# Performance work log

Measured on AMD Instinct MI355X. Metric: run time of the kernel, lower is better.

## Reference

```python
import jax, jax.numpy as jnp
import numpy as np
from jax import lax

N_FREE = 10
DT = 0.1
COMP = 4


def setup_inputs() -> dict:
    key = jax.random.key(0)
    kx, kw = jax.random.split(key)
    B, D = 256, 16384
    nodes = D // COMP  # 4096
    x = jax.random.normal(kx, (B, D), dtype=jnp.float32)
    # Hopfield-style node-coupling matrix (learned parameter), small init for stable relaxation
    W = jax.random.normal(kw, (nodes, nodes), dtype=jnp.float32) * 0.02
    return {"x": x, "W": W}


def reference(x, W):
    B, D = x.shape
    nodes = D // COMP
    # project scalar features to multivectors (B, nodes, comp)
    x_mv = x.reshape(B, nodes, COMP)
    W_sym = 0.5 * (W + W.T)  # symmetric coupling => well-defined energy

    def step(h, _):
        rho = jnp.tanh(h)                                      # (B, nodes, comp)
        drive = jnp.einsum('nm,bmc->bnc', W_sym, rho) + x_mv   # recurrent + input coupling
        grad_E = h - (1.0 - rho * rho) * drive                 # dE/dh
        return h - DT * grad_E, None

    h_free, _ = lax.scan(step, x_mv, None, length=N_FREE)
    return h_free[..., 0]  # scalar (grade-0) component, (B, nodes)
```

## Files before the change

### kernel.cpp

```cpp
#include <hip/hip_runtime.h>
#include <hip/hip_bf16.h>


#define NODES 4096
#define KDIM  4096
#define MDIM  1024
#define DLEN  16384
#define HALF_ELEMS 4194304

typedef __attribute__((ext_vector_type(8))) __bf16 bf16x8;
typedef __attribute__((ext_vector_type(8))) unsigned short u16x8;
typedef __attribute__((ext_vector_type(4))) float  f32x4;

static __device__ __forceinline__ unsigned short f32_to_bf16(float f) {
    unsigned int u = __float_as_uint(f);
    u += 0x7fffu + ((u >> 16) & 1u);
    return (unsigned short)(u >> 16);
}
static __device__ __forceinline__ float bf16_to_f32(unsigned short u) {
    return __uint_as_float(((unsigned int)u) << 16);
}

__global__ __launch_bounds__(256)
void symw_kernel(const float* __restrict__ W, unsigned short* __restrict__ Wbp) {
    __shared__ float Ta[64][64];
    __shared__ float Tb[64][65];
    const int tn = blockIdx.y, tm = blockIdx.x;
    const int c  = threadIdx.x & 63;
    const int r0 = threadIdx.x >> 6;
#pragma unroll
    for (int rr = 0; rr < 16; ++rr) {
        int r = r0 * 16 + rr;
        Ta[r][c] = W[(size_t)(tn * 64 + r) * 4096 + tm * 64 + c];
        Tb[r][c] = W[(size_t)(tm * 64 + r) * 4096 + tn * 64 + c];
    }
    __syncthreads();
#pragma unroll
    for (int rr = 0; rr < 16; ++rr) {
        int r = r0 * 16 + rr;
        float v = 0.5f * (Ta[r][c] + Tb[c][r]);
        int n = tn * 64 + r;
        int k = tm * 64 + c;
        size_t addr = ((size_t)(k >> 5) * 256 + (n >> 4)) * 512
                    + (size_t)((n & 15) | (((k >> 3) & 3) << 4)) * 8 + (k & 7);
        Wbp[addr] = f32_to_bf16(v);
    }
}

__global__ __launch_bounds__(256)
void init_kernel(const float* __restrict__ x, float* __restrict__ h,
                 unsigned short* __restrict__ P0) {
    int idx = blockIdx.x * blockDim.x + threadIdx.x;
    int b = idx >> 12;
    int m = idx & 4095;
    f32x4 xv = *(const f32x4*)(x + (size_t)idx * 4);
    *(f32x4*)(h + (size_t)idx * 4) = xv;
    size_t base = ((size_t)(m >> 5) * 64 + (b >> 2)) * 512
                + (size_t)((m >> 3) & 3) * 128 + (m & 7);
#pragma unroll
    for (int c = 0; c < 4; ++c) {
        P0[base + (size_t)((b & 3) * 4 + c) * 8] = f32_to_bf16(tanhf(xv[c]));
    }
}

__global__ __launch_bounds__(256, 4)
void gemm_kernel(const unsigned short* __restrict__ Pcur,
                 const unsigned short* __restrict__ Wbp,
                 unsigned short* __restrict__ Dp) {
    __shared__ unsigned short Bs[4 * 4096];

    const int id   = blockIdx.x;
    const int bx   = (id & 7) * 4 + ((id >> 3) & 3);
    const int by   = (id >> 5) & 7;
    const int ks   = id >> 8;
    const int T0   = ks * 32;

    const int tid  = threadIdx.x;
    const int w    = tid >> 6;
    const int lane = tid & 63;
    const int wm   = w >> 1;
    const int wn   = w & 1;

    size_t soff[2]; int dsto[2];
#pragma unroll
    for (int j = 0; j < 2; ++j) {
        int c = tid + 256 * j;
        soff[j] = ((size_t)(bx * 8 + (c >> 6))) * 512 + (size_t)(c & 63) * 8;
        dsto[j] = c * 8;
    }
    size_t aoff[4];
#pragma unroll
    for (int mi = 0; mi < 4; ++mi)
        aoff[mi] = ((size_t)(by * 8 + wm * 4 + mi)) * 512 + (size_t)lane * 8;
    const int boff = (wn * 4) * 512 + lane * 8;

    f32x4 acc[4][4];
#pragma unroll
    for (int mi = 0; mi < 4; ++mi)
#pragma unroll
        for (int ni = 0; ni < 4; ++ni)
            acc[mi][ni] = (f32x4){0.f, 0.f, 0.f, 0.f};

    bf16x8 aA[4], aB[4];

#define TC(t) ((t) < 31 ? (t) : 31)

#define STAGE(slot, tl)                                                         \
    do {                                                                        \
        const unsigned short* src = Wbp + (size_t)(T0 + (tl)) * 131072;         \
        _Pragma("unroll")                                                       \
        for (int j = 0; j < 2; ++j) {                                           \
            __builtin_amdgcn_global_load_lds(                                   \
                (const __attribute__((address_space(1))) void*)(src + soff[j]), \
                (__attribute__((address_space(3))) void*)                      \
                    (Bs + (slot) * 4096 + dsto[j]),                             \
                16, 0, 0);                                                      \
        }                                                                       \
    } while (0)

#define LOADA(s, tl)                                                            \
    do {                                                                        \
        const unsigned short* Pt = Pcur + (size_t)(T0 + (tl)) * 32768;          \
        _Pragma("unroll")                                                       \
        for (int mi = 0; mi < 4; ++mi)                                          \
            s[mi] = *(const bf16x8*)(Pt + aoff[mi]);                            \
    } while (0)

#define COMPUTE(slot, s)                                                        \
    do {                                                                        \
        const unsigned short* Bb = Bs + (slot) * 4096;                          \
        bf16x8 bfr[4];                                                          \
        _Pragma("unroll")                                                       \
        for (int ni = 0; ni < 4; ++ni)                                          \
            bfr[ni] = *(const bf16x8*)(Bb + boff + ni * 512);                   \
        _Pragma("unroll")                                                       \
        for (int mi = 0; mi < 4; ++mi)                                          \
            _Pragma("unroll")                                                   \
            for (int ni = 0; ni < 4; ++ni)                                      \
                acc[mi][ni] = __builtin_amdgcn_mfma_f32_16x16x32_bf16(          \
                    s[mi], bfr[ni], acc[mi][ni], 0, 0, 0);                      \
    } while (0)

    STAGE(0, 0);
    LOADA(aA, 0);
    STAGE(1, 1);
    STAGE(2, 2);
    LOADA(aB, 1);
    STAGE(3, 3);
    asm volatile("s_waitcnt vmcnt(10)" ::: "memory");
    __builtin_amdgcn_s_barrier();
    COMPUTE(0, aA);

    for (int tp = 0; tp < 15; ++tp) {
        const int t = 1 + 2 * tp;
        LOADA(aA, TC(t + 1));
        STAGE((t + 3) & 3, TC(t + 3));
        asm volatile("s_waitcnt vmcnt(10)" ::: "memory");
        __builtin_amdgcn_s_barrier();
        COMPUTE(t & 3, aB);

        const int u = t + 1;
        LOADA(aB, TC(u + 1));
        STAGE((u + 3) & 3, TC(u + 3));
        asm volatile("s_waitcnt vmcnt(10)" ::: "memory");
        __builtin_amdgcn_s_barrier();
        COMPUTE(u & 3, aA);
    }
    asm volatile("s_waitcnt vmcnt(0)" ::: "memory");
    __builtin_amdgcn_s_barrier();
    COMPUTE(31 & 3, aB);
#undef STAGE
#undef LOADA
#undef COMPUTE
#undef TC

    const int lr = lane & 15, lk = lane >> 4;
    unsigned short* D = Dp + (size_t)ks * HALF_ELEMS;
#pragma unroll
    for (int mi = 0; mi < 4; ++mi) {
        int i0 = by * 128 + wm * 64 + mi * 16 + lk * 4;
#pragma unroll
        for (int ni = 0; ni < 4; ++ni) {
            int n = bx * 128 + wn * 64 + ni * 16 + lr;
#pragma unroll
            for (int r = 0; r < 4; ++r)
                D[(size_t)(i0 + r) * NODES + n] = f32_to_bf16(acc[mi][ni][r]);
        }
    }
}

__global__ __launch_bounds__(256)
void combine_kernel(const unsigned short* __restrict__ Dp,
                    const float* __restrict__ x,
                    float* __restrict__ h,
                    unsigned short* __restrict__ Pnxt,
                    float* __restrict__ out) {
    int g  = blockIdx.x * 256 + threadIdx.x;
    int b  = g >> 9;
    int mg = (g & 511) << 3;
    size_t hbase = (size_t)b * DLEN + (size_t)mg * 4;

    f32x4 hv[8], xv[8];
#pragma unroll
    for (int e = 0; e < 8; ++e) {
        hv[e] = *(const f32x4*)(h + hbase + e * 4);
        xv[e] = *(const f32x4*)(x + hbase + e * 4);
    }
    u16x8 d0[4], d1[4], d2[4], d3[4];
#pragma unroll
    for (int c = 0; c < 4; ++c) {
        size_t off = (size_t)(b * 4 + c) * NODES + mg;
        d0[c] = *(const u16x8*)(Dp + off);
        d1[c] = *(const u16x8*)(Dp + HALF_ELEMS + off);
        d2[c] = *(const u16x8*)(Dp + 2 * (size_t)HALF_ELEMS + off);
        d3[c] = *(const u16x8*)(Dp + 3 * (size_t)HALF_ELEMS + off);
    }
    u16x8 pn[4];
    float o[8];
#pragma unroll
    for (int e = 0; e < 8; ++e) {
#pragma unroll
        for (int c = 0; c < 4; ++c) {
            float p = (bf16_to_f32(d0[c][e]) + bf16_to_f32(d1[c][e]))
                    + (bf16_to_f32(d2[c][e]) + bf16_to_f32(d3[c][e]));
            float hvv  = hv[e][c];
            float rho  = tanhf(hvv);
            float drive = p + xv[e][c];
            float hnew = 0.9f * hvv + 0.1f * (1.0f - rho * rho) * drive;
            hv[e][c] = hnew;
            pn[c][e] = f32_to_bf16(tanhf(hnew));
            if (c == 0) o[e] = hnew;
        }
    }
    if (Pnxt) {
#pragma unroll
        for (int e = 0; e < 8; ++e)
            *(f32x4*)(h + hbase + e * 4) = hv[e];
#pragma unroll
        for (int c = 0; c < 4; ++c) {
            size_t pa = (size_t)(mg >> 5) * 32768 + (size_t)(b >> 2) * 512
                      + (size_t)(((b & 3) * 4 + c) | (((mg >> 3) & 3) << 4)) * 8;
            *(u16x8*)(Pnxt + pa) = pn[c];
        }
    }
    if (out) {
        *(f32x4*)(out + (size_t)b * NODES + mg)     = (f32x4){o[0], o[1], o[2], o[3]};
        *(f32x4*)(out + (size_t)b * NODES + mg + 4) = (f32x4){o[4], o[5], o[6], o[7]};
    }
}

extern "C" void kernel_launch(void* const* d_in, const int* in_sizes, int n_in,
                              void* d_out, int out_size, void* d_ws, size_t ws_size,
                              hipStream_t stream) {
    const float* x = (const float*)d_in[0];
    const float* W = (const float*)d_in[1];
    float* out = (float*)d_out;

    char* ws = (char*)d_ws;
    unsigned short* Wbp = (unsigned short*)(ws);
    unsigned short* P0  = (unsigned short*)(ws + ((size_t)32 << 20));
    unsigned short* P1  = (unsigned short*)(ws + ((size_t)40 << 20));
    float*          h   = (float*)(ws + ((size_t)48 << 20));
    unsigned short* Dp  = (unsigned short*)(ws + ((size_t)64 << 20));

    symw_kernel<<<dim3(64, 64), 256, 0, stream>>>(W, Wbp);
    init_kernel<<<dim3(4096), 256, 0, stream>>>(x, h, P0);

    unsigned short* pc = P0;
    unsigned short* pn = P1;
    for (int s = 0; s < 10; ++s) {
        gemm_kernel<<<dim3(1024), 256, 0, stream>>>(pc, Wbp, Dp);
        combine_kernel<<<dim3(512), 256, 0, stream>>>(
            Dp, x, h, (s == 9) ? nullptr : pn, (s == 9) ? out : nullptr);
        unsigned short* t = pc; pc = pn; pn = t;
    }
}
```

Baseline: 645.8 us.

## Restructure GEMM to 512-thread blocks with 2-way split-K and triple-buffered LDS

The GEMM moves from 1024 blocks of 256 threads with 4-way split-K to 256 blocks of 512 threads with 2-way split-K. Each block now covers a 256-row tile, and each stage loads two K-slices into a triple-buffered LDS ring. MFMA phases are wrapped in s_setprio, and the combine kernel now sums two partials instead of four. The aim is to cut partial-sum traffic and raise reuse per block. The cost is exactly one block per CU (256 blocks), which gives less latency hiding and a longer serial K loop.

Result: faster. 618.4 us (-4.2%).

```diff
diff --git a/kernel.cpp b/kernel.cpp
--- a/kernel.cpp
+++ b/kernel.cpp
@@ -63,17 +63,16 @@
     }
 }
 
-__global__ __launch_bounds__(256, 4)
+__global__ __launch_bounds__(512, 1)
 void gemm_kernel(const unsigned short* __restrict__ Pcur,
                  const unsigned short* __restrict__ Wbp,
                  unsigned short* __restrict__ Dp) {
-    __shared__ unsigned short Bs[4 * 4096];
-
-    const int id   = blockIdx.x;
-    const int bx   = (id & 7) * 4 + ((id >> 3) & 3);
-    const int by   = (id >> 5) & 7;
-    const int ks   = id >> 8;
-    const int T0   = ks * 32;
+    __shared__ unsigned short Bs[3 * 8192];
+
+    const int id = blockIdx.x;
+    const int bx = (id & 7) | (((id >> 5) & 3) << 3);
+    const int by = (id >> 3) & 3;
+    const int ks = id >> 7;
 
     const int tid  = threadIdx.x;
     const int w    = tid >> 6;
@@ -81,18 +80,18 @@
     const int wm   = w >> 1;
     const int wn   = w & 1;
 
-    size_t soff[2]; int dsto[2];
+    size_t soff[2];
 #pragma unroll
     for (int j = 0; j < 2; ++j) {
-        int c = tid + 256 * j;
-        soff[j] = ((size_t)(bx * 8 + (c >> 6))) * 512 + (size_t)(c & 63) * 8;
-        dsto[j] = c * 8;
+        int c  = tid + 512 * j;
+        int f  = c >> 6;
+        int kf = f >> 3, nf = f & 7;
+        soff[j] = ((size_t)kf * 256 + bx * 8 + nf) * 512 + (size_t)(c & 63) * 8;
     }
     size_t aoff[4];
 #pragma unroll
     for (int mi = 0; mi < 4; ++mi)
-        aoff[mi] = ((size_t)(by * 8 + wm * 4 + mi)) * 512 + (size_t)lane * 8;
-    const int boff = (wn * 4) * 512 + lane * 8;
+        aoff[mi] = ((size_t)(by * 16 + wm * 4 + mi)) * 512 + (size_t)lane * 8;
 
     f32x4 acc[4][4];
 #pragma unroll
@@ -101,84 +100,90 @@
         for (int ni = 0; ni < 4; ++ni)
             acc[mi][ni] = (f32x4){0.f, 0.f, 0.f, 0.f};
 
-    bf16x8 aA[4], aB[4];
-
-#define TC(t) ((t) < 31 ? (t) : 31)
-
-#define STAGE(slot, tl)                                                         \
+    bf16x8 aE[4][2], aO[4][2];
+
+#define STAGE(slot, t)                                                          \
     do {                                                                        \
-        const unsigned short* src = Wbp + (size_t)(T0 + (tl)) * 131072;         \
+        const unsigned short* src = Wbp + (size_t)(ks * 64 + 2 * (t)) * 131072; \
         _Pragma("unroll")                                                       \
         for (int j = 0; j < 2; ++j) {                                           \
+            int c = tid + 512 * j;                                              \
             __builtin_amdgcn_global_load_lds(                                   \
                 (const __attribute__((address_space(1))) void*)(src + soff[j]), \
                 (__attribute__((address_space(3))) void*)                      \
-                    (Bs + (slot) * 4096 + dsto[j]),                             \
+                    (Bs + (slot) * 8192 + c * 8),                               \
                 16, 0, 0);                                                      \
         }                                                                       \
     } while (0)
 
-#define LOADA(s, tl)                                                            \
+#define LOADA(s, t)                                                             \
     do {                                                                        \
-        const unsigned short* Pt = Pcur + (size_t)(T0 + (tl)) * 32768;          \
-        _Pragma("unroll")                                                       \
-        for (int mi = 0; mi < 4; ++mi)                                          \
-            s[mi] = *(const bf16x8*)(Pt + aoff[mi]);                            \
-    } while (0)
-
-#define COMPUTE(slot, s)                                                        \
-    do {                                                                        \
-        const unsigned short* Bb = Bs + (slot) * 4096;                          \
-        bf16x8 bfr[4];                                                          \
-        _Pragma("unroll")                                                       \
-        for (int ni = 0; ni < 4; ++ni)                                          \
-            bfr[ni] = *(const bf16x8*)(Bb + boff + ni * 512);                   \
+        const unsigned short* Pt = Pcur + (size_t)(ks * 64 + 2 * (t)) * 32768;  \
         _Pragma("unroll")                                                       \
         for (int mi = 0; mi < 4; ++mi)                                          \
             _Pragma("unroll")                                                   \
-            for (int ni = 0; ni < 4; ++ni)                                      \
-                acc[mi][ni] = __builtin_amdgcn_mfma_f32_16x16x32_bf16(          \
-                    s[mi], bfr[ni], acc[mi][ni], 0, 0, 0);                      \
+            for (int kk = 0; kk < 2; ++kk)                                      \
+                s[mi][kk] = *(const bf16x8*)(Pt + (size_t)kk * 32768 + aoff[mi]); \
     } while (0)
 
+#define PHASE(slot, p, s)                                                       \
+    do {                                                                        \
+        bf16x8 bq[2][2];                                                        \
+        _Pragma("unroll")                                                       \
+        for (int i = 0; i < 2; ++i)                                             \
+            _Pragma("unroll")                                                   \
+            for (int kk = 0; kk < 2; ++kk)                                      \
+                bq[i][kk] = *(const bf16x8*)(Bs + (slot) * 8192                 \
+                    + (kk * 8 + wn * 4 + (p) * 2 + i) * 512 + lane * 8);        \
+        __builtin_amdgcn_s_setprio(1);                                          \
+        _Pragma("unroll")                                                       \
+        for (int mi = 0; mi < 4; ++mi)                                          \
+            _Pragma("unroll")                                                   \
+            for (int i = 0; i < 2; ++i)                                         \
+                _Pragma("unroll")                                               \
+                for (int kk = 0; kk < 2; ++kk)                                  \
+                    acc[mi][(p) * 2 + i] = __builtin_amdgcn_mfma_f32_16x16x32_bf16( \
+                        s[mi][kk], bq[i][kk], acc[mi][(p) * 2 + i], 0, 0, 0);   \
+        __builtin_amdgcn_s_setprio(0);                                          \
+    } while (0)
+
     STAGE(0, 0);
-    LOADA(aA, 0);
     STAGE(1, 1);
-    STAGE(2, 2);
-    LOADA(aB, 1);
-    STAGE(3, 3);
+    LOADA(aE, 0);
+
+    for (int tp = 0; tp < 15; ++tp) {
+        const int t = 2 * tp;
+        asm volatile("s_waitcnt vmcnt(10)" ::: "memory");
+        asm volatile("s_barrier" ::: "memory");
+        STAGE((t + 2) % 3, t + 2);
+        LOADA(aO, t + 1);
+        PHASE(t % 3, 0, aE);
+        PHASE(t % 3, 1, aE);
+        asm volatile("s_waitcnt vmcnt(10)" ::: "memory");
+        asm volatile("s_barrier" ::: "memory");
+        STAGE((t + 3) % 3, t + 3);
+        LOADA(aE, t + 2);
+        PHASE((t + 1) % 3, 0, aO);
+        PHASE((t + 1) % 3, 1, aO);
+    }
     asm volatile("s_waitcnt vmcnt(10)" ::: "memory");
-    __builtin_amdgcn_s_barrier();
-    COMPUTE(0, aA);
-
-    for (int tp = 0; tp < 15; ++tp) {
-        const int t = 1 + 2 * tp;
-        LOADA(aA, TC(t + 1));
-        STAGE((t + 3) & 3, TC(t + 3));
-        asm volatile("s_waitcnt vmcnt(10)" ::: "memory");
-        __builtin_amdgcn_s_barrier();
-        COMPUTE(t & 3, aB);
-
-        const int u = t + 1;
-        LOADA(aB, TC(u + 1));
-        STAGE((u + 3) & 3, TC(u + 3));
-        asm volatile("s_waitcnt vmcnt(10)" ::: "memory");
-        __builtin_amdgcn_s_barrier();
-        COMPUTE(u & 3, aA);
-    }
-    asm volatile("s_waitcnt vmcnt(0)" ::: "memory");
-    __builtin_amdgcn_s_barrier();
-    COMPUTE(31 & 3, aB);
+    asm volatile("s_barrier" ::: "memory");
+    LOADA(aO, 31);
+    PHASE(0, 0, aE);
+    PHASE(0, 1, aE);
+    asm volatile("s_waitcnt vmcnt(8)" ::: "memory");
+    asm volatile("s_barrier" ::: "memory");
+    PHASE(1, 0, aO);
+    PHASE(1, 1, aO);
 #undef STAGE
 #undef LOADA
-#undef COMPUTE
-#undef TC
+#undef PHASE
 
     const int lr = lane & 15, lk = lane >> 4;
     unsigned short* D = Dp + (size_t)ks * HALF_ELEMS;
 #pragma unroll
     for (int mi = 0; mi < 4; ++mi) {
-        int i0 = by * 128 + wm * 64 + mi * 16 + lk * 4;
+        int i0 = by * 256 + wm * 64 + mi * 16 + lk * 4;
 #pragma unroll
         for (int ni = 0; ni < 4; ++ni) {
             int n = bx * 128 + wn * 64 + ni * 16 + lr;
@@ -206,14 +211,12 @@
         hv[e] = *(const f32x4*)(h + hbase + e * 4);
         xv[e] = *(const f32x4*)(x + hbase + e * 4);
     }
-    u16x8 d0[4], d1[4], d2[4], d3[4];
+    u16x8 d0[4], d1[4];
 #pragma unroll
     for (int c = 0; c < 4; ++c) {
         size_t off = (size_t)(b * 4 + c) * NODES + mg;
         d0[c] = *(const u16x8*)(Dp + off);
         d1[c] = *(const u16x8*)(Dp + HALF_ELEMS + off);
-        d2[c] = *(const u16x8*)(Dp + 2 * (size_t)HALF_ELEMS + off);
-        d3[c] = *(const u16x8*)(Dp + 3 * (size_t)HALF_ELEMS + off);
     }
     u16x8 pn[4];
     float o[8];
@@ -221,8 +224,7 @@
     for (int e = 0; e < 8; ++e) {
 #pragma unroll
         for (int c = 0; c < 4; ++c) {
-            float p = (bf16_to_f32(d0[c][e]) + bf16_to_f32(d1[c][e]))
-                    + (bf16_to_f32(d2[c][e]) + bf16_to_f32(d3[c][e]));
+            float p    = bf16_to_f32(d0[c][e]) + bf16_to_f32(d1[c][e]);
             float hvv  = hv[e][c];
             float rho  = tanhf(hvv);
             float drive = p + xv[e][c];
@@ -269,7 +271,7 @@
     unsigned short* pc = P0;
     unsigned short* pn = P1;
     for (int s = 0; s < 10; ++s) {
-        gemm_kernel<<<dim3(1024), 256, 0, stream>>>(pc, Wbp, Dp);
+        gemm_kernel<<<dim3(256), 512, 0, stream>>>(pc, Wbp, Dp);
         combine_kernel<<<dim3(512), 256, 0, stream>>>(
             Dp, x, h, (s == 9) ? nullptr : pn, (s == 9) ? out : nullptr);
         unsigned short* t = pc; pc = pn; pn = t;
```
